# Kernel tuning notes

Measured on AMD Instinct MI355X. Metric: run time of the kernel, lower is better.

Reference implementation:

```python
import jax, jax.numpy as jnp
import numpy as np

MARGIN = 1.0  # init kwarg 'margin'
N, D = 8192, 128
NUM_CLASSES = 100

def setup_inputs() -> dict:
    key = jax.random.key(0)
    kx, ky = jax.random.split(key)
    x = jax.random.normal(kx, (N, D), dtype=jnp.float32)
    y = jax.random.randint(ky, (N,), 0, NUM_CLASSES, dtype=jnp.int64)
    return {"x": x, "y": y}

def reference(x, y):
    # Squared euclidean pairwise distances: d[i,j] = sum_k (x[i,k] - x[j,k])^2
    # computed via the ||a||^2 + ||b||^2 - 2 a.b expansion to avoid an NxNxD
    # intermediate. Clamp tiny negatives from fp roundoff.
    sq = jnp.sum(x * x, axis=-1)                      # [N]
    d = sq[:, None] + sq[None, :] - 2.0 * (x @ x.T)   # [N, N]
    d = jnp.maximum(d, 0.0)
    same = (y[:, None] == y[None, :]).astype(x.dtype)  # [N, N] positive-pair mask
    # Faithful to the torch module: dissimilar pairs contribute d, similar
    # pairs contribute hinge clamp(margin - d, 0); mean over all N*N pairs.
    loss = jnp.mean((1.0 - same) * d + same * jnp.maximum(MARGIN - d, 0.0))
    return loss
```

## Files before the change

kernel.cpp:

```cpp
#include <hip/hip_runtime.h>


#define N_ROWS 8192
#define DIM    128
#define NCLS   100
#define CAP    224
#define SB     256
#define SROWS  (N_ROWS / SB)
#define GBPC   4
#define GRAMB  (NCLS * GBPC)

typedef _Float16 half8  __attribute__((ext_vector_type(8)));
typedef _Float16 half4v __attribute__((ext_vector_type(4)));
typedef float    float4v __attribute__((ext_vector_type(4)));

__global__ __launch_bounds__(256) void scan_kernel(
    const float* __restrict__ x, const int* __restrict__ y,
    _Float16* __restrict__ gh, float* __restrict__ sqg, int* __restrict__ cnt,
    float* __restrict__ Scol, float* __restrict__ SQc)
{
    const int b = blockIdx.x, tid = threadIdx.x;
    const int l = tid & 31, g = tid >> 5;
    const float4* x4 = (const float4*)x;
    float4 ca = make_float4(0.f, 0.f, 0.f, 0.f);
    __shared__ float4 colred[256];

    #pragma unroll
    for (int pass = 0; pass < SROWS / 8; ++pass) {
        const int r = b * SROWS + pass * 8 + g;
        float4 v = x4[r * 32 + l];
        ca.x += v.x; ca.y += v.y; ca.z += v.z; ca.w += v.w;
        float s = v.x*v.x + v.y*v.y + v.z*v.z + v.w*v.w;
        s += __shfl_xor(s, 1);  s += __shfl_xor(s, 2);  s += __shfl_xor(s, 4);
        s += __shfl_xor(s, 8);  s += __shfl_xor(s, 16);
        const int c = y[r];
        int p = 0;
        if (l == 0) p = atomicAdd(&cnt[c], 1);
        p = __shfl(p, 0, 32);
        if (p < CAP) {
            half4v h;
            h[0] = (_Float16)v.x; h[1] = (_Float16)v.y;
            h[2] = (_Float16)v.z; h[3] = (_Float16)v.w;
            *(half4v*)(gh + (size_t)(c * CAP + p) * DIM + l * 4) = h;
            if (l == 0) sqg[c * CAP + p] = s;
        }
        if (l == 0) atomicAdd(&SQc[c], s);
    }
    colred[tid] = ca;
    __syncthreads();
    if (tid < 32) {
        float4 a = colred[tid];
        #pragma unroll
        for (int gg = 1; gg < 8; ++gg) {
            float4 t = colred[tid + 32 * gg];
            a.x += t.x; a.y += t.y; a.z += t.z; a.w += t.w;
        }
        atomicAdd(&Scol[4 * tid + 0], a.x);
        atomicAdd(&Scol[4 * tid + 1], a.y);
        atomicAdd(&Scol[4 * tid + 2], a.z);
        atomicAdd(&Scol[4 * tid + 3], a.w);
    }
}

__global__ __launch_bounds__(256) void gram_kernel(
    const _Float16* __restrict__ gh, const float* __restrict__ sqg,
    const int* __restrict__ cnt, const float* __restrict__ Scol,
    const float* __restrict__ SQc,
    float* __restrict__ Hsum, float* __restrict__ SSsum,
    int* __restrict__ done, float* __restrict__ out)
{
    const int c = blockIdx.x >> 2, qq = blockIdx.x & 3, tid = threadIdx.x;
    __shared__ float sqm[CAP];
    __shared__ float wred[8];
    __shared__ int   lastFlag;

    const int mtrue = cnt[c];
    const int m = mtrue < CAP ? mtrue : CAP;
    const int ntiles = (m + 15) >> 4;
    const int ntp = ntiles * (ntiles + 1) / 2;

    if (tid < CAP) sqm[tid] = (tid < m) ? sqg[c * CAP + tid] : 0.f;
    __syncthreads();

    const int wave = tid >> 6, lane = tid & 63;
    const int lr = lane & 15, q = lane >> 4;
    float hacc = 0.f, dsum = 0.f;
    const _Float16* base = gh + (size_t)c * CAP * DIM;

    for (int tp = qq * 4 + wave; tp < ntp; tp += 16) {
        int ta = 0, rem = tp;
        while (rem >= ntiles - ta) { rem -= ntiles - ta; ++ta; }
        const int tb = ta + rem;
        const half8* ap = (const half8*)(base + (ta * 16 + lr) * DIM + q * 8);
        const half8* bp = (const half8*)(base + (tb * 16 + lr) * DIM + q * 8);
        float4v acc = {0.f, 0.f, 0.f, 0.f};
        #pragma unroll
        for (int kb = 0; kb < 4; ++kb)
            acc = __builtin_amdgcn_mfma_f32_16x16x32_f16(ap[kb * 4], bp[kb * 4], acc, 0, 0, 0);
        const float w = (ta == tb) ? 1.f : 2.f;
        #pragma unroll
        for (int i = 0; i < 4; ++i) {
            const int a  = ta * 16 + q * 4 + i;
            const int bb = tb * 16 + lr;
            if (a < m && bb < m) {
                const float dot = acc[i];
                dsum += w * dot;
                if (a != bb) {
                    float d = fmaxf(sqm[a] + sqm[bb] - 2.f * dot, 0.f);
                    hacc += w * fmaxf(1.f - d, 0.f);
                }
            }
        }
    }
    #pragma unroll
    for (int off = 32; off > 0; off >>= 1) {
        hacc += __shfl_xor(hacc, off);
        dsum += __shfl_xor(dsum, off);
    }
    if (lane == 0) { wred[wave] = hacc; wred[4 + wave] = dsum; }
    __syncthreads();
    if (tid == 0) {
        float h = wred[0] + wred[1] + wred[2] + wred[3];
        float d = wred[4] + wred[5] + wred[6] + wred[7];
        if (h != 0.f) atomicAdd(Hsum, h);
        atomicAdd(SSsum, d);
        __threadfence();
        int p = atomicAdd(done, 1);
        lastFlag = (p == GRAMB - 1);
    }
    __syncthreads();
    if (!lastFlag) return;

    __threadfence();
    const double Nf = (double)N_ROWS;
    double contrib = 0.0;
    if (tid < DIM)  { double v = Scol[tid]; contrib -= 2.0 * v * v; }
    if (tid < NCLS) {
        double qv = SQc[tid];
        contrib += 2.0 * qv * (Nf - (double)cnt[tid]);
    }
    if (tid == 0) {
        float H  = __hip_atomic_load(Hsum,  __ATOMIC_RELAXED, __HIP_MEMORY_SCOPE_AGENT);
        float SS = __hip_atomic_load(SSsum, __ATOMIC_RELAXED, __HIP_MEMORY_SCOPE_AGENT);
        contrib += 2.0 * (double)SS + (double)H + Nf * 1.0 ;
    }
    __shared__ double dred[256];
    dred[tid] = contrib;
    __syncthreads();
    for (int s = 128; s > 0; s >>= 1) {
        if (tid < s) dred[tid] += dred[tid + s];
        __syncthreads();
    }
    if (tid == 0) out[0] = (float)(dred[0] / (Nf * Nf));
}

extern "C" void kernel_launch(void* const* d_in, const int* in_sizes, int n_in,
                              void* d_out, int out_size, void* d_ws, size_t ws_size,
                              hipStream_t stream) {
    const float* x = (const float*)d_in[0];
    const int*   y = (const int*)d_in[1];

    _Float16* gh = (_Float16*)d_ws;
    float* sqg   = (float*)(gh + (size_t)NCLS * CAP * DIM);
    float* Scol  = sqg + NCLS * CAP;
    float* SQc   = Scol + DIM;
    float* Hsum  = SQc + NCLS;
    float* SSsum = Hsum + 1;
    int*   cnt   = (int*)(SSsum + 1);
    int*   done  = cnt + NCLS;
    const size_t zero_words = DIM + NCLS + 2 + NCLS + 1;

    hipMemsetAsync(Scol, 0, zero_words * sizeof(float), stream);
    scan_kernel<<<SB,    256, 0, stream>>>(x, y, gh, sqg, cnt, Scol, SQc);
    gram_kernel<<<GRAMB, 256, 0, stream>>>(gh, sqg, cnt, Scol, SQc,
                                           Hsum, SSsum, done, (float*)d_out);
}
```

Baseline: 110.6 us.

## Split class ranking into its own kernel, widen scan and gram grids, replicate atomics

Adds a rank_kernel that counts class membership in shared memory first and then issues one global atomic per class per block. This takes the serial per-row global atomicAdd out of the scan. The scan kernel then processes one row per warp across 1024 blocks, and its column and class sums are spread over 8 replicas to reduce atomic contention. The gram kernel uses 8 blocks per class instead of 4 and reads squared norms directly from global memory instead of staging them in LDS. This adds one more kernel launch, and the final reduction now sums the replicas in float.

```diff
diff --git a/kernel.cpp b/kernel.cpp
--- a/kernel.cpp
+++ b/kernel.cpp
@@ -5,48 +5,61 @@
 #define DIM    128
 #define NCLS   100
 #define CAP    224
-#define SB     256
-#define SROWS  (N_ROWS / SB)
-#define GBPC   4
+#define RB     32
+#define SCB    1024
+#define GBPC   8
 #define GRAMB  (NCLS * GBPC)
+#define NREP   8
 
 typedef _Float16 half8  __attribute__((ext_vector_type(8)));
 typedef _Float16 half4v __attribute__((ext_vector_type(4)));
 typedef float    float4v __attribute__((ext_vector_type(4)));
 
+__global__ __launch_bounds__(256) void rank_kernel(
+    const int* __restrict__ y, int* __restrict__ cnt, int* __restrict__ rank)
+{
+    const int tid = threadIdx.x, r = blockIdx.x * 256 + tid;
+    __shared__ int lcnt[NCLS], lbase[NCLS];
+    if (tid < NCLS) lcnt[tid] = 0;
+    __syncthreads();
+    const int c = y[r];
+    const int intra = atomicAdd(&lcnt[c], 1);
+    __syncthreads();
+    if (tid < NCLS && lcnt[tid] > 0)
+        lbase[tid] = atomicAdd(&cnt[tid], lcnt[tid]);
+    __syncthreads();
+    rank[r] = lbase[c] + intra;
+}
+
 __global__ __launch_bounds__(256) void scan_kernel(
     const float* __restrict__ x, const int* __restrict__ y,
-    _Float16* __restrict__ gh, float* __restrict__ sqg, int* __restrict__ cnt,
-    float* __restrict__ Scol, float* __restrict__ SQc)
+    const int* __restrict__ rank,
+    _Float16* __restrict__ gh, float* __restrict__ sqg,
+    float* __restrict__ Scol8, float* __restrict__ SQc8)
 {
     const int b = blockIdx.x, tid = threadIdx.x;
     const int l = tid & 31, g = tid >> 5;
+    const int r = b * 8 + g;
+    const int rep = b & (NREP - 1);
     const float4* x4 = (const float4*)x;
-    float4 ca = make_float4(0.f, 0.f, 0.f, 0.f);
     __shared__ float4 colred[256];
 
-    #pragma unroll
-    for (int pass = 0; pass < SROWS / 8; ++pass) {
-        const int r = b * SROWS + pass * 8 + g;
-        float4 v = x4[r * 32 + l];
-        ca.x += v.x; ca.y += v.y; ca.z += v.z; ca.w += v.w;
-        float s = v.x*v.x + v.y*v.y + v.z*v.z + v.w*v.w;
-        s += __shfl_xor(s, 1);  s += __shfl_xor(s, 2);  s += __shfl_xor(s, 4);
-        s += __shfl_xor(s, 8);  s += __shfl_xor(s, 16);
-        const int c = y[r];
-        int p = 0;
-        if (l == 0) p = atomicAdd(&cnt[c], 1);
-        p = __shfl(p, 0, 32);
-        if (p < CAP) {
-            half4v h;
-            h[0] = (_Float16)v.x; h[1] = (_Float16)v.y;
-            h[2] = (_Float16)v.z; h[3] = (_Float16)v.w;
-            *(half4v*)(gh + (size_t)(c * CAP + p) * DIM + l * 4) = h;
-            if (l == 0) sqg[c * CAP + p] = s;
-        }
-        if (l == 0) atomicAdd(&SQc[c], s);
+    float4 v = x4[r * 32 + l];
+    float s = v.x*v.x + v.y*v.y + v.z*v.z + v.w*v.w;
+    s += __shfl_xor(s, 1);  s += __shfl_xor(s, 2);  s += __shfl_xor(s, 4);
+    s += __shfl_xor(s, 8);  s += __shfl_xor(s, 16);
+    const int c = y[r];
+    const int p = rank[r];
+    if (p < CAP) {
+        half4v h;
+        h[0] = (_Float16)v.x; h[1] = (_Float16)v.y;
+        h[2] = (_Float16)v.z; h[3] = (_Float16)v.w;
+        *(half4v*)(gh + (size_t)(c * CAP + p) * DIM + l * 4) = h;
+        if (l == 0) sqg[c * CAP + p] = s;
     }
-    colred[tid] = ca;
+    if (l == 0) atomicAdd(&SQc8[rep * NCLS + c], s);
+
+    colred[tid] = v;
     __syncthreads();
     if (tid < 32) {
         float4 a = colred[tid];
@@ -55,22 +68,22 @@
             float4 t = colred[tid + 32 * gg];
             a.x += t.x; a.y += t.y; a.z += t.z; a.w += t.w;
         }
-        atomicAdd(&Scol[4 * tid + 0], a.x);
-        atomicAdd(&Scol[4 * tid + 1], a.y);
-        atomicAdd(&Scol[4 * tid + 2], a.z);
-        atomicAdd(&Scol[4 * tid + 3], a.w);
+        float* dst = Scol8 + rep * DIM;
+        atomicAdd(&dst[4 * tid + 0], a.x);
+        atomicAdd(&dst[4 * tid + 1], a.y);
+        atomicAdd(&dst[4 * tid + 2], a.z);
+        atomicAdd(&dst[4 * tid + 3], a.w);
     }
 }
 
 __global__ __launch_bounds__(256) void gram_kernel(
     const _Float16* __restrict__ gh, const float* __restrict__ sqg,
-    const int* __restrict__ cnt, const float* __restrict__ Scol,
-    const float* __restrict__ SQc,
+    const int* __restrict__ cnt,
+    const float* __restrict__ Scol8, const float* __restrict__ SQc8,
     float* __restrict__ Hsum, float* __restrict__ SSsum,
     int* __restrict__ done, float* __restrict__ out)
 {
-    const int c = blockIdx.x >> 2, qq = blockIdx.x & 3, tid = threadIdx.x;
-    __shared__ float sqm[CAP];
+    const int c = blockIdx.x >> 3, qq = blockIdx.x & 7, tid = threadIdx.x;
     __shared__ float wred[8];
     __shared__ int   lastFlag;
 
@@ -79,15 +92,13 @@
     const int ntiles = (m + 15) >> 4;
     const int ntp = ntiles * (ntiles + 1) / 2;
 
-    if (tid < CAP) sqm[tid] = (tid < m) ? sqg[c * CAP + tid] : 0.f;
-    __syncthreads();
-
     const int wave = tid >> 6, lane = tid & 63;
     const int lr = lane & 15, q = lane >> 4;
     float hacc = 0.f, dsum = 0.f;
     const _Float16* base = gh + (size_t)c * CAP * DIM;
+    const float* sqb_ = sqg + c * CAP;
 
-    for (int tp = qq * 4 + wave; tp < ntp; tp += 16) {
+    for (int tp = qq * 4 + wave; tp < ntp; tp += 32) {
         int ta = 0, rem = tp;
         while (rem >= ntiles - ta) { rem -= ntiles - ta; ++ta; }
         const int tb = ta + rem;
@@ -98,15 +109,16 @@
         for (int kb = 0; kb < 4; ++kb)
             acc = __builtin_amdgcn_mfma_f32_16x16x32_f16(ap[kb * 4], bp[kb * 4], acc, 0, 0, 0);
         const float w = (ta == tb) ? 1.f : 2.f;
+        const int bb = tb * 16 + lr;
+        const float sqb = (bb < m) ? sqb_[bb] : 0.f;
         #pragma unroll
         for (int i = 0; i < 4; ++i) {
-            const int a  = ta * 16 + q * 4 + i;
-            const int bb = tb * 16 + lr;
+            const int a = ta * 16 + q * 4 + i;
             if (a < m && bb < m) {
                 const float dot = acc[i];
                 dsum += w * dot;
                 if (a != bb) {
-                    float d = fmaxf(sqm[a] + sqm[bb] - 2.f * dot, 0.f);
+                    float d = fmaxf(sqb_[a] + sqb - 2.f * dot, 0.f);
                     hacc += w * fmaxf(1.f - d, 0.f);
                 }
             }
@@ -123,7 +135,7 @@
         float h = wred[0] + wred[1] + wred[2] + wred[3];
         float d = wred[4] + wred[5] + wred[6] + wred[7];
         if (h != 0.f) atomicAdd(Hsum, h);
-        atomicAdd(SSsum, d);
+        if (d != 0.f) atomicAdd(SSsum, d);
         __threadfence();
         int p = atomicAdd(done, 1);
         lastFlag = (p == GRAMB - 1);
@@ -134,10 +146,17 @@
     __threadfence();
     const double Nf = (double)N_ROWS;
     double contrib = 0.0;
-    if (tid < DIM)  { double v = Scol[tid]; contrib -= 2.0 * v * v; }
+    if (tid < DIM) {
+        float sc = 0.f;
+        #pragma unroll
+        for (int k = 0; k < NREP; ++k) sc += Scol8[k * DIM + tid];
+        contrib -= 2.0 * (double)sc * (double)sc;
+    }
     if (tid < NCLS) {
-        double qv = SQc[tid];
-        contrib += 2.0 * qv * (Nf - (double)cnt[tid]);
+        float qv = 0.f;
+        #pragma unroll
+        for (int k = 0; k < NREP; ++k) qv += SQc8[k * NCLS + tid];
+        contrib += 2.0 * (double)qv * (Nf - (double)cnt[tid]);
     }
     if (tid == 0) {
         float H  = __hip_atomic_load(Hsum,  __ATOMIC_RELAXED, __HIP_MEMORY_SCOPE_AGENT);
@@ -162,16 +181,18 @@
 
     _Float16* gh = (_Float16*)d_ws;
     float* sqg   = (float*)(gh + (size_t)NCLS * CAP * DIM);
-    float* Scol  = sqg + NCLS * CAP;
-    float* SQc   = Scol + DIM;
-    float* Hsum  = SQc + NCLS;
+    int*   rank  = (int*)(sqg + NCLS * CAP);
+    float* Scol8 = (float*)(rank + N_ROWS);
+    float* SQc8  = Scol8 + NREP * DIM;
+    float* Hsum  = SQc8 + NREP * NCLS;
     float* SSsum = Hsum + 1;
     int*   cnt   = (int*)(SSsum + 1);
     int*   done  = cnt + NCLS;
-    const size_t zero_words = DIM + NCLS + 2 + NCLS + 1;
+    const size_t zero_words = NREP * DIM + NREP * NCLS + 2 + NCLS + 1;
 
-    hipMemsetAsync(Scol, 0, zero_words * sizeof(float), stream);
-    scan_kernel<<<SB,    256, 0, stream>>>(x, y, gh, sqg, cnt, Scol, SQc);
-    gram_kernel<<<GRAMB, 256, 0, stream>>>(gh, sqg, cnt, Scol, SQc,
+    hipMemsetAsync(Scol8, 0, zero_words * sizeof(float), stream);
+    rank_kernel<<<RB,    256, 0, stream>>>(y, cnt, rank);
+    scan_kernel<<<SCB,   256, 0, stream>>>(x, y, rank, gh, sqg, Scol8, SQc8);
+    gram_kernel<<<GRAMB, 256, 0, stream>>>(gh, sqg, cnt, Scol8, SQc8,
                                            Hsum, SSsum, done, (float*)d_out);
 }
```

Result: faster. 97.74 us (-11.7%).
